# Performance work log

Hardware: AMD Instinct MI355X
Metric: run time of the kernel (lower is better)

Reference implementation:

```python
import jax, jax.numpy as jnp
import numpy as np

D_MODEL = 512
NUM_HEADS = 8
DEPTH = D_MODEL // NUM_HEADS


def setup_inputs() -> dict:
    key = jax.random.key(0)
    kx, kq, kk, kv, ko = jax.random.split(key, 5)
    scale = 1.0 / np.sqrt(D_MODEL)
    return {
        "x": jax.random.normal(kx, (4, 2048, D_MODEL), dtype=jnp.float32),
        "W_q": jax.random.normal(kq, (D_MODEL, D_MODEL), dtype=jnp.float32) * scale,
        "W_k": jax.random.normal(kk, (D_MODEL, D_MODEL), dtype=jnp.float32) * scale,
        "W_v": jax.random.normal(kv, (D_MODEL, D_MODEL), dtype=jnp.float32) * scale,
        "W_o": jax.random.normal(ko, (D_MODEL, D_MODEL), dtype=jnp.float32) * scale,
    }


def reference(x, W_q, W_k, W_v, W_o):
    B, S, _ = x.shape
    # nn.Linear with weight W: y = x @ W.T
    def split_heads(t):
        return t.reshape(B, S, NUM_HEADS, DEPTH).transpose(0, 2, 1, 3)  # [B,H,S,D]
    Q = split_heads(x @ W_q.T)
    K = split_heads(x @ W_k.T)
    V = split_heads(x @ W_v.T)
    b = -jnp.log(jnp.asarray(S, dtype=jnp.float32))  # -log(seq_len) bias
    inv_sqrt_dk = 1.0 / jnp.sqrt(jnp.asarray(DEPTH, dtype=jnp.float32))
    qk = jnp.einsum('bhqd,bhkd->bhqk', Q, K) * inv_sqrt_dk
    attn = jax.nn.sigmoid(qk + b)  # non-softmax sigmoid attention
    out = jnp.einsum('bhqk,bhkd->bhqd', attn, V)
    out = out.transpose(0, 2, 1, 3).reshape(B, S, D_MODEL)
    return out @ W_o.T
```

## Files before the change

### kernel.cpp

```cpp
#include <hip/hip_runtime.h>
#include <stdint.h>

typedef _Float16 f16x8 __attribute__((ext_vector_type(8)));
typedef _Float16 f16x4 __attribute__((ext_vector_type(4)));
typedef __fp16 h16x2 __attribute__((ext_vector_type(2)));
typedef float f32x4 __attribute__((ext_vector_type(4)));
typedef float f32x16 __attribute__((ext_vector_type(16)));

#define SEQ 2048
#define NHEADS 8

#define GLOAD_LDS16(gp, lp)                                                        \
  __builtin_amdgcn_global_load_lds(                                                \
      (const __attribute__((address_space(1))) void*)(uintptr_t)(const void*)(gp), \
      (__attribute__((address_space(3))) void*)(uintptr_t)(void*)(lp), 16, 0, 0)

#define DSR(dst, base, off) \
  asm volatile("ds_read_b128 %0, %1 offset:%c2" : "=v"(dst) : "v"(base), "i"(off))

#define WAIT_LGKM(n)                                         \
  do {                                                       \
    asm volatile("s_waitcnt lgkmcnt(%c0)" ::"i"(n) : "memory"); \
    __builtin_amdgcn_sched_barrier(0);                       \
  } while (0)

__device__ __forceinline__ void barrier_lds() {
  __builtin_amdgcn_s_waitcnt(0xc07f);
  __builtin_amdgcn_s_barrier();
}

__device__ __forceinline__ f16x4 pack4(float a, float b, float c, float d) {
  h16x2 lo = __builtin_amdgcn_cvt_pkrtz(a, b);
  h16x2 hi = __builtin_amdgcn_cvt_pkrtz(c, d);
  f16x4 o;
  o.x = (_Float16)lo.x; o.y = (_Float16)lo.y;
  o.z = (_Float16)hi.x; o.w = (_Float16)hi.y;
  return o;
}

__global__ void cvt_all_kernel(const float* __restrict__ x, const float* __restrict__ wq,
                               const float* __restrict__ wk, const float* __restrict__ wv,
                               const float* __restrict__ wo, _Float16* __restrict__ xh,
                               _Float16* __restrict__ wh) {
  int i = blockIdx.x * 256 + threadIdx.x;
  const float* src;
  _Float16* dst;
  int off;
  if (i < 1048576) {
    src = x; dst = xh; off = i;
  } else {
    int j = i - 1048576;
    int sel = j >> 16;
    off = j & 65535;
    src = (sel == 0) ? wq : (sel == 1) ? wk : (sel == 2) ? wv : wo;
    dst = wh + (size_t)sel * 262144;
  }
  float4 v = ((const float4*)src)[off];
  ((f16x4*)dst)[off] = pack4(v.x, v.y, v.z, v.w);
}

__device__ __forceinline__ void gemm_tile_bt(const _Float16* __restrict__ A,
                                             const _Float16* __restrict__ B,
                                             int m0, int n0,
                                             _Float16* lds,
                                             f32x4 (&acc)[4][4]) {
  const int tid = threadIdx.x;
  const int w = tid >> 6, lane = tid & 63;
  const int wr = w >> 1, wc = w & 1;
  const int lrow = lane & 15, q = lane >> 4;
  const int snb = w * 32 + (lane >> 3);
  const int scb = lane & 7;

#pragma unroll
  for (int i = 0; i < 4; ++i)
#pragma unroll
    for (int j = 0; j < 4; ++j)
#pragma unroll
      for (int r = 0; r < 4; ++r) acc[i][j][r] = 0.f;

#pragma unroll
  for (int t = 0; t < 4; ++t) {
    int n = snb + t * 8;
    int cbg = scb ^ (n & 7);
    GLOAD_LDS16(A + (size_t)(m0 + n) * 512 + cbg * 8, lds + (w * 32 + t * 8) * 64);
    GLOAD_LDS16(B + (size_t)(n0 + n) * 512 + cbg * 8, lds + 8192 + (w * 32 + t * 8) * 64);
  }

  for (int kt = 0; kt < 8; ++kt) {
    __syncthreads();
    if (kt < 7) {
      _Float16* nb = lds + ((kt + 1) & 1) * 16384;
#pragma unroll
      for (int t = 0; t < 4; ++t) {
        int n = snb + t * 8;
        int cbg = scb ^ (n & 7);
        GLOAD_LDS16(A + (size_t)(m0 + n) * 512 + (kt + 1) * 64 + cbg * 8, nb + (w * 32 + t * 8) * 64);
        GLOAD_LDS16(B + (size_t)(n0 + n) * 512 + (kt + 1) * 64 + cbg * 8, nb + 8192 + (w * 32 + t * 8) * 64);
      }
    }
    _Float16* As = lds + (kt & 1) * 16384;
    _Float16* Bs = As + 8192;

    f16x8 af[4][2], bfr[4][2];
#pragma unroll
    for (int i = 0; i < 4; ++i) {
      int m = wr * 64 + i * 16 + lrow;
#pragma unroll
      for (int kk = 0; kk < 2; ++kk) {
        int cb = (kk * 4 + q) ^ (m & 7);
        af[i][kk] = *(const f16x8*)(As + m * 64 + cb * 8);
      }
    }
#pragma unroll
    for (int j = 0; j < 4; ++j) {
      int n = wc * 64 + j * 16 + lrow;
#pragma unroll
      for (int kk = 0; kk < 2; ++kk) {
        int cb = (kk * 4 + q) ^ (n & 7);
        bfr[j][kk] = *(const f16x8*)(Bs + n * 64 + cb * 8);
      }
    }
#pragma unroll
    for (int i = 0; i < 4; ++i)
#pragma unroll
      for (int j = 0; j < 4; ++j) {
        acc[i][j] = __builtin_amdgcn_mfma_f32_16x16x32_f16(af[i][0], bfr[j][0], acc[i][j], 0, 0, 0);
        acc[i][j] = __builtin_amdgcn_mfma_f32_16x16x32_f16(af[i][1], bfr[j][1], acc[i][j], 0, 0, 0);
      }
  }
}

__global__ __launch_bounds__(256, 2) void qkv_kernel(
    const _Float16* __restrict__ xb, const _Float16* __restrict__ Wq,
    const _Float16* __restrict__ Wk, const _Float16* __restrict__ Wv,
    _Float16* __restrict__ Qo, _Float16* __restrict__ Ko, _Float16* __restrict__ Vto) {
  __shared__ _Float16 pool[32768];
  const int z = blockIdx.z;
  f32x4 acc[4][4];
  const int tid = threadIdx.x, w = tid >> 6, lane = tid & 63;
  const int wr = w >> 1, wc = w & 1, lcol = lane & 15, q = lane >> 4;

  if (z < 2) {
    const int m0 = blockIdx.y * 128;
    const int n0 = blockIdx.x * 128;
    gemm_tile_bt((z == 0) ? Wq : Wk, xb, m0, n0, pool, acc);
    _Float16* outp = (z == 0) ? Qo : Ko;
    __syncthreads();
#pragma unroll
    for (int i = 0; i < 4; ++i) {
      int cl = wr * 64 + i * 16 + q * 4;
#pragma unroll
      for (int j = 0; j < 4; ++j) {
        int s = wc * 64 + j * 16 + lcol;
        *(f16x4*)(pool + s * 136 + cl) =
            pack4(acc[i][j][0], acc[i][j][1], acc[i][j][2], acc[i][j][3]);
      }
    }
    __syncthreads();
#pragma unroll
    for (int it = 0; it < 16; ++it) {
      int srow = it * 8 + (tid >> 5);
      int ch = tid & 31;
      f16x4 v = *(const f16x4*)(pool + srow * 136 + ch * 4);
      *(f16x4*)(outp + (size_t)(n0 + srow) * 512 + m0 + ch * 4) = v;
    }
  } else {
    const int m0 = blockIdx.x * 128;
    const int n0 = blockIdx.y * 128;
    gemm_tile_bt(xb, Wv, m0, n0, pool, acc);
    const int bb = m0 >> 11, sl0 = m0 & 2047;
    __syncthreads();
#pragma unroll
    for (int i = 0; i < 4; ++i) {
      int s0 = wr * 64 + i * 16 + q * 4;
#pragma unroll
      for (int j = 0; j < 4; ++j) {
        int c = wc * 64 + j * 16 + lcol;
        *(f16x4*)(pool + c * 136 + s0) =
            pack4(acc[i][j][0], acc[i][j][1], acc[i][j][2], acc[i][j][3]);
      }
    }
    __syncthreads();
#pragma unroll
    for (int it = 0; it < 16; ++it) {
      int crow = it * 8 + (tid >> 5);
      int ch = tid & 31;
      int cg = n0 + crow, h = cg >> 6, d = cg & 63;
      f16x4 v = *(const f16x4*)(pool + crow * 136 + ch * 4);
      *(f16x4*)(Vto + ((size_t)((bb * NHEADS + h) * 64 + d)) * SEQ + sl0 + ch * 4) = v;
    }
  }
}

__device__ __forceinline__ void attn_window(
    f16x8 k0, f16x8 k1, f16x8 k2, f16x8 k3,
    f16x8 v00, f16x8 v01, f16x8 v10, f16x8 v11,
    const f16x8 (&qb)[4], const f32x16& z16, f32x16& o0, f32x16& o1) {
  const float c1 = 0.18033688011112042f;
  __builtin_amdgcn_s_setprio(1);
  f32x16 s = __builtin_amdgcn_mfma_f32_32x32x16_f16(k0, qb[0], z16, 0, 0, 0);
  s = __builtin_amdgcn_mfma_f32_32x32x16_f16(k1, qb[1], s, 0, 0, 0);
  s = __builtin_amdgcn_mfma_f32_32x32x16_f16(k2, qb[2], s, 0, 0, 0);
  s = __builtin_amdgcn_mfma_f32_32x32x16_f16(k3, qb[3], s, 0, 0, 0);
  __builtin_amdgcn_s_setprio(0);

  float p[16];
#pragma unroll
  for (int r = 0; r < 16; ++r) {
    float wp = __builtin_amdgcn_exp2f(__builtin_fmaf(s[r], c1, -1.0f));
    float e = wp * 0.0009765625f;
    p[r] = __builtin_fmaf(wp, __builtin_fmaf(e, e, -e), wp);
  }

  f16x8 pa0, pa1;
  {
    h16x2 a0 = __builtin_amdgcn_cvt_pkrtz(p[0], p[1]);
    h16x2 a1 = __builtin_amdgcn_cvt_pkrtz(p[2], p[3]);
    h16x2 a2 = __builtin_amdgcn_cvt_pkrtz(p[4], p[5]);
    h16x2 a3 = __builtin_amdgcn_cvt_pkrtz(p[6], p[7]);
    pa0[0] = (_Float16)a0.x; pa0[1] = (_Float16)a0.y;
    pa0[2] = (_Float16)a1.x; pa0[3] = (_Float16)a1.y;
    pa0[4] = (_Float16)a2.x; pa0[5] = (_Float16)a2.y;
    pa0[6] = (_Float16)a3.x; pa0[7] = (_Float16)a3.y;
    h16x2 b0 = __builtin_amdgcn_cvt_pkrtz(p[8], p[9]);
    h16x2 b1 = __builtin_amdgcn_cvt_pkrtz(p[10], p[11]);
    h16x2 b2 = __builtin_amdgcn_cvt_pkrtz(p[12], p[13]);
    h16x2 b3 = __builtin_amdgcn_cvt_pkrtz(p[14], p[15]);
    pa1[0] = (_Float16)b0.x; pa1[1] = (_Float16)b0.y;
    pa1[2] = (_Float16)b1.x; pa1[3] = (_Float16)b1.y;
    pa1[4] = (_Float16)b2.x; pa1[5] = (_Float16)b2.y;
    pa1[6] = (_Float16)b3.x; pa1[7] = (_Float16)b3.y;
  }

  __builtin_amdgcn_s_setprio(1);
  o0 = __builtin_amdgcn_mfma_f32_32x32x16_f16(pa0, v00, o0, 0, 0, 0);
  o1 = __builtin_amdgcn_mfma_f32_32x32x16_f16(pa0, v01, o1, 0, 0, 0);
  o0 = __builtin_amdgcn_mfma_f32_32x32x16_f16(pa1, v10, o0, 0, 0, 0);
  o1 = __builtin_amdgcn_mfma_f32_32x32x16_f16(pa1, v11, o1, 0, 0, 0);
  __builtin_amdgcn_s_setprio(0);
}

#define KT_BODY(BUFB, NBUFB, PF)                                              \
  {                                                                           \
    __syncthreads();                                                          \
    if (PF) {                                                                 \
      _Float16* nb = (_Float16*)((char*)lds + (NBUFB));                       \
      GLOAD_LDS16(kgb + koff[0], nb + (w * 16) * 64);                         \
      GLOAD_LDS16(kgb + koff[1], nb + (w * 16 + 8) * 64);                     \
      GLOAD_LDS16(vgb + voff[0], nb + 4096 + (w * 16) * 64);                  \
      GLOAD_LDS16(vgb + voff[1], nb + 4096 + (w * 16 + 8) * 64);              \
      kgb += 65536;                                                           \
      vgb += 128;                                                             \
    }                                                                         \
    f16x8 kA0, kA1, kA2, kA3, vA00, vA01, vA10, vA11;                         \
    f16x8 kB0, kB1, kB2, kB3, vB00, vB01, vB10, vB11;                         \
    DSR(kA0, kb0, (BUFB));                                                    \
    DSR(kA1, kb1, (BUFB));                                                    \
    DSR(kA2, kb2, (BUFB));                                                    \
    DSR(kA3, kb3, (BUFB));                                                    \
    DSR(vA00, pv00, (BUFB) + 8192);                                           \
    DSR(vA01, pv00, (BUFB) + 12288);                                          \
    DSR(vA10, pv01, (BUFB) + 8192);                                           \
    DSR(vA11, pv01, (BUFB) + 12288);                                          \
    DSR(kB0, kb0, (BUFB) + 4096);                                             \
    DSR(kB1, kb1, (BUFB) + 4096);                                             \
    DSR(kB2, kb2, (BUFB) + 4096);                                             \
    DSR(kB3, kb3, (BUFB) + 4096);                                             \
    DSR(vB00, pv10, (BUFB) + 8192);                                           \
    DSR(vB01, pv10, (BUFB) + 12288);                                          \
    DSR(vB10, pv11, (BUFB) + 8192);                                           \
    DSR(vB11, pv11, (BUFB) + 12288);                                          \
    WAIT_LGKM(8);                                                             \
    attn_window(kA0, kA1, kA2, kA3, vA00, vA01, vA10, vA11, qb, z16, oacc0, oacc1); \
    WAIT_LGKM(0);                                                             \
    attn_window(kB0, kB1, kB2, kB3, vB00, vB01, vB10, vB11, qb, z16, oacc0, oacc1); \
  }

__global__ __launch_bounds__(256, 2) void attn_kernel(
    const _Float16* __restrict__ Qw, const _Float16* __restrict__ Kw,
    const _Float16* __restrict__ Vtw, _Float16* __restrict__ Ow) {
  __shared__ _Float16 lds[16384];

  const int tid = threadIdx.x, w = tid >> 6, lane = tid & 63;
  const int q31 = lane & 31, hi = lane >> 5;

  const int L = blockIdx.x;
  const int xcd = L & 7, slot = L >> 3;
  const int bh = xcd * 4 + (slot >> 4), qt = slot & 15;
  const int b = bh >> 3, h = bh & 7;
  const int q0 = qt * 128;

  const _Float16* Qp = Qw + ((size_t)(b * SEQ + q0)) * 512 + h * 64;
  const _Float16* Kp = Kw + ((size_t)b * SEQ) * 512 + h * 64;
  const _Float16* Vp = Vtw + (size_t)bh * 64 * SEQ;

  const int l3 = lane >> 3, l7 = lane & 7;

  int koff[2], voff[2];
#pragma unroll
  for (int t = 0; t < 2; ++t) {
    int n = w * 16 + t * 8 + l3;
    int cbg = l7 ^ l3 ^ ((t & 1) << 2);
    koff[t] = n * 1024 + cbg * 16;
    voff[t] = n * 4096 + cbg * 16;
  }
  const char* kgb = (const char*)Kp;
  const char* vgb = (const char*)Vp;

  _Float16* Qs = lds + 8192;
#pragma unroll
  for (int t = 0; t < 4; ++t) {
    int n = w * 32 + t * 8 + l3;
    int cbg = l7 ^ l3 ^ ((t & 1) << 2);
    GLOAD_LDS16((const char*)Qp + n * 1024 + cbg * 16, Qs + (w * 32 + t * 8) * 64);
  }
  GLOAD_LDS16(kgb + koff[0], lds + (w * 16) * 64);
  GLOAD_LDS16(kgb + koff[1], lds + (w * 16 + 8) * 64);
  GLOAD_LDS16(vgb + voff[0], lds + 4096 + (w * 16) * 64);
  GLOAD_LDS16(vgb + voff[1], lds + 4096 + (w * 16 + 8) * 64);
  kgb += 65536;
  vgb += 128;
  __syncthreads();

  const int fq = (q31 & 7) ^ (((q31 >> 3) & 1) << 2);
  const int klp = (q31 & 3) | ((q31 & 4) << 1) | ((q31 & 8) >> 1) | (q31 & 16);
  const int fk = (klp & 7) ^ (((klp >> 3) & 1) << 2);

  f16x8 qb[4];
  const int qrow = w * 32 + q31;
#pragma unroll
  for (int s = 0; s < 4; ++s) {
    int cb = (s * 2 + hi) ^ fq;
    qb[s] = *(const f16x8*)(Qs + qrow * 64 + cb * 8);
  }

  const int kb0 = klp * 128 + (((0 * 2 + hi) ^ fk) << 4);
  const int kb1 = klp * 128 + (((1 * 2 + hi) ^ fk) << 4);
  const int kb2 = klp * 128 + (((2 * 2 + hi) ^ fk) << 4);
  const int kb3 = klp * 128 + (((3 * 2 + hi) ^ fk) << 4);
  const int pv00 = q31 * 128 + (((0 + 0 + hi) ^ fq) << 4);
  const int pv01 = q31 * 128 + (((0 + 2 + hi) ^ fq) << 4);
  const int pv10 = q31 * 128 + (((4 + 0 + hi) ^ fq) << 4);
  const int pv11 = q31 * 128 + (((4 + 2 + hi) ^ fq) << 4);

  f32x16 oacc0, oacc1, z16;
#pragma unroll
  for (int r = 0; r < 16; ++r) { z16[r] = 0.f; oacc0[r] = 0.f; oacc1[r] = 0.f; }

  for (int p = 0; p < 16; ++p) {
    KT_BODY(0, 16384, true);
    KT_BODY(16384, 0, (p < 15));
  }

  barrier_lds();
  _Float16* Ob = lds;
#pragma unroll
  for (int t = 0; t < 2; ++t) {
#pragma unroll
    for (int r = 0; r < 16; ++r) {
      int row = w * 32 + (r & 3) + ((r >> 2) << 3) + hi * 4;
      int d = t * 32 + q31;
      float v = (t == 0) ? oacc0[r] : oacc1[r];
      Ob[row * 72 + d] = (_Float16)(v * 0.0009765625f);
    }
  }
  barrier_lds();
#pragma unroll
  for (int it = 0; it < 8; ++it) {
    int row = it * 16 + (tid >> 4);
    int ch = tid & 15;
    f16x4 v = *(const f16x4*)(Ob + row * 72 + ch * 4);
    *(f16x4*)(Ow + (size_t)(b * SEQ + q0 + row) * 512 + h * 64 + ch * 4) = v;
  }
}

__global__ __launch_bounds__(256, 2) void oproj_kernel(
    const _Float16* __restrict__ A, const _Float16* __restrict__ Wo,
    float* __restrict__ out) {
  __shared__ _Float16 pool[32768];
  const int m0 = blockIdx.x * 128, n0 = blockIdx.y * 128;
  f32x4 acc[4][4];
  gemm_tile_bt(A, Wo, m0, n0, pool, acc);

  const int tid = threadIdx.x, w = tid >> 6, lane = tid & 63;
  const int wr = w >> 1, wc = w & 1, lcol = lane & 15, q = lane >> 4;
#pragma unroll
  for (int i = 0; i < 4; ++i) {
    int gm0 = m0 + wr * 64 + i * 16 + q * 4;
#pragma unroll
    for (int j = 0; j < 4; ++j) {
      int gn = n0 + wc * 64 + j * 16 + lcol;
#pragma unroll
      for (int r = 0; r < 4; ++r)
        out[(size_t)(gm0 + r) * 512 + gn] = acc[i][j][r];
    }
  }
}

extern "C" void kernel_launch(void* const* d_in, const int* in_sizes, int n_in,
                              void* d_out, int out_size, void* d_ws, size_t ws_size,
                              hipStream_t stream) {
  const float* x = (const float*)d_in[0];
  const float* Wq = (const float*)d_in[1];
  const float* Wk = (const float*)d_in[2];
  const float* Wv = (const float*)d_in[3];
  const float* Wo = (const float*)d_in[4];
  float* out = (float*)d_out;
  char* ws = (char*)d_ws;

  _Float16* xh = (_Float16*)(ws + 0);
  _Float16* wh = (_Float16*)(ws + 8388608);
  _Float16* Qw = (_Float16*)(ws + 10485760);
  _Float16* Kw = (_Float16*)(ws + 18874368);
  _Float16* Vtw = (_Float16*)(ws + 27262976);
  _Float16* Ow = (_Float16*)(ws + 35651584);

  _Float16* wqh = wh;
  _Float16* wkh = wh + 262144;
  _Float16* wvh = wh + 524288;
  _Float16* woh = wh + 786432;

  cvt_all_kernel<<<5120, 256, 0, stream>>>(x, Wq, Wk, Wv, Wo, xh, wh);
  qkv_kernel<<<dim3(64, 4, 3), 256, 0, stream>>>(xh, wqh, wkh, wvh, Qw, Kw, Vtw);
  attn_kernel<<<512, 256, 0, stream>>>(Qw, Kw, Vtw, Ow);
  oproj_kernel<<<dim3(64, 4), 256, 0, stream>>>(Ow, woh, out);
}
```

Baseline: 149.8 us.

## Load attention K/V tiles directly from global into registers, bypassing LDS

The attention kernel no longer stages K and V tiles through double-buffered LDS with block-wide barriers. Each wave now issues global_load_dwordx4 straight into registers for two ping-pong windows and waits on vmcnt. This removes the per-tile __syncthreads and the LDS round trip, and shrinks LDS use. In exchange every wave fetches its own K/V copy from global/L2, so redundant traffic rises across the 4 waves, and latency hiding now depends on how far ahead the register double-buffering prefetches.

```diff
diff --git a/kernel.cpp b/kernel.cpp
--- a/kernel.cpp
+++ b/kernel.cpp
@@ -15,19 +15,14 @@
       (const __attribute__((address_space(1))) void*)(uintptr_t)(const void*)(gp), \
       (__attribute__((address_space(3))) void*)(uintptr_t)(void*)(lp), 16, 0, 0)
 
-#define DSR(dst, base, off) \
-  asm volatile("ds_read_b128 %0, %1 offset:%c2" : "=v"(dst) : "v"(base), "i"(off))
-
-#define WAIT_LGKM(n)                                         \
-  do {                                                       \
-    asm volatile("s_waitcnt lgkmcnt(%c0)" ::"i"(n) : "memory"); \
-    __builtin_amdgcn_sched_barrier(0);                       \
+#define GLD16(dst, ptr, imm) \
+  asm volatile("global_load_dwordx4 %0, %1, off offset:%c2" : "=&v"(dst) : "v"(ptr), "i"(imm))
+
+#define VMW(n)                                                     \
+  do {                                                             \
+    asm volatile("s_waitcnt vmcnt(%c0)" ::"i"(n) : "memory");      \
+    __builtin_amdgcn_sched_barrier(0);                             \
   } while (0)
-
-__device__ __forceinline__ void barrier_lds() {
-  __builtin_amdgcn_s_waitcnt(0xc07f);
-  __builtin_amdgcn_s_barrier();
-}
 
 __device__ __forceinline__ f16x4 pack4(float a, float b, float c, float d) {
   h16x2 lo = __builtin_amdgcn_cvt_pkrtz(a, b);
@@ -192,16 +187,15 @@
   }
 }
 
-__device__ __forceinline__ void attn_window(
-    f16x8 k0, f16x8 k1, f16x8 k2, f16x8 k3,
-    f16x8 v00, f16x8 v01, f16x8 v10, f16x8 v11,
-    const f16x8 (&qb)[4], const f32x16& z16, f32x16& o0, f32x16& o1) {
+__device__ __forceinline__ void attn_window(const f16x8 (&ka)[4], const f16x8 (&vb)[4],
+                                            const f16x8 (&qb)[4], const f32x16& z16,
+                                            f32x16& o0, f32x16& o1) {
   const float c1 = 0.18033688011112042f;
   __builtin_amdgcn_s_setprio(1);
-  f32x16 s = __builtin_amdgcn_mfma_f32_32x32x16_f16(k0, qb[0], z16, 0, 0, 0);
-  s = __builtin_amdgcn_mfma_f32_32x32x16_f16(k1, qb[1], s, 0, 0, 0);
-  s = __builtin_amdgcn_mfma_f32_32x32x16_f16(k2, qb[2], s, 0, 0, 0);
-  s = __builtin_amdgcn_mfma_f32_32x32x16_f16(k3, qb[3], s, 0, 0, 0);
+  f32x16 s = __builtin_amdgcn_mfma_f32_32x32x16_f16(ka[0], qb[0], z16, 0, 0, 0);
+  s = __builtin_amdgcn_mfma_f32_32x32x16_f16(ka[1], qb[1], s, 0, 0, 0);
+  s = __builtin_amdgcn_mfma_f32_32x32x16_f16(ka[2], qb[2], s, 0, 0, 0);
+  s = __builtin_amdgcn_mfma_f32_32x32x16_f16(ka[3], qb[3], s, 0, 0, 0);
   __builtin_amdgcn_s_setprio(0);
 
   float p[16];
@@ -233,55 +227,34 @@
   }
 
   __builtin_amdgcn_s_setprio(1);
-  o0 = __builtin_amdgcn_mfma_f32_32x32x16_f16(pa0, v00, o0, 0, 0, 0);
-  o1 = __builtin_amdgcn_mfma_f32_32x32x16_f16(pa0, v01, o1, 0, 0, 0);
-  o0 = __builtin_amdgcn_mfma_f32_32x32x16_f16(pa1, v10, o0, 0, 0, 0);
-  o1 = __builtin_amdgcn_mfma_f32_32x32x16_f16(pa1, v11, o1, 0, 0, 0);
+  o0 = __builtin_amdgcn_mfma_f32_32x32x16_f16(pa0, vb[0], o0, 0, 0, 0);
+  o1 = __builtin_amdgcn_mfma_f32_32x32x16_f16(pa0, vb[1], o1, 0, 0, 0);
+  o0 = __builtin_amdgcn_mfma_f32_32x32x16_f16(pa1, vb[2], o0, 0, 0, 0);
+  o1 = __builtin_amdgcn_mfma_f32_32x32x16_f16(pa1, vb[3], o1, 0, 0, 0);
   __builtin_amdgcn_s_setprio(0);
 }
 
-#define KT_BODY(BUFB, NBUFB, PF)                                              \
-  {                                                                           \
-    __syncthreads();                                                          \
-    if (PF) {                                                                 \
-      _Float16* nb = (_Float16*)((char*)lds + (NBUFB));                       \
-      GLOAD_LDS16(kgb + koff[0], nb + (w * 16) * 64);                         \
-      GLOAD_LDS16(kgb + koff[1], nb + (w * 16 + 8) * 64);                     \
-      GLOAD_LDS16(vgb + voff[0], nb + 4096 + (w * 16) * 64);                  \
-      GLOAD_LDS16(vgb + voff[1], nb + 4096 + (w * 16 + 8) * 64);              \
-      kgb += 65536;                                                           \
-      vgb += 128;                                                             \
-    }                                                                         \
-    f16x8 kA0, kA1, kA2, kA3, vA00, vA01, vA10, vA11;                         \
-    f16x8 kB0, kB1, kB2, kB3, vB00, vB01, vB10, vB11;                         \
-    DSR(kA0, kb0, (BUFB));                                                    \
-    DSR(kA1, kb1, (BUFB));                                                    \
-    DSR(kA2, kb2, (BUFB));                                                    \
-    DSR(kA3, kb3, (BUFB));                                                    \
-    DSR(vA00, pv00, (BUFB) + 8192);                                           \
-    DSR(vA01, pv00, (BUFB) + 12288);                                          \
-    DSR(vA10, pv01, (BUFB) + 8192);                                           \
-    DSR(vA11, pv01, (BUFB) + 12288);                                          \
-    DSR(kB0, kb0, (BUFB) + 4096);                                             \
-    DSR(kB1, kb1, (BUFB) + 4096);                                             \
-    DSR(kB2, kb2, (BUFB) + 4096);                                             \
-    DSR(kB3, kb3, (BUFB) + 4096);                                             \
-    DSR(vB00, pv10, (BUFB) + 8192);                                           \
-    DSR(vB01, pv10, (BUFB) + 12288);                                          \
-    DSR(vB10, pv11, (BUFB) + 8192);                                           \
-    DSR(vB11, pv11, (BUFB) + 12288);                                          \
-    WAIT_LGKM(8);                                                             \
-    attn_window(kA0, kA1, kA2, kA3, vA00, vA01, vA10, vA11, qb, z16, oacc0, oacc1); \
-    WAIT_LGKM(0);                                                             \
-    attn_window(kB0, kB1, kB2, kB3, vB00, vB01, vB10, vB11, qb, z16, oacc0, oacc1); \
-  }
+#define ISSUE_WIN(KA, VB, KP, VP0, VP1) \
+  do {                                  \
+    GLD16(KA[0], KP, 0);                \
+    GLD16(KA[1], KP, 32);               \
+    GLD16(KA[2], KP, 64);               \
+    GLD16(KA[3], KP, 96);               \
+    GLD16(VB[0], VP0, 0);               \
+    GLD16(VB[1], VP1, 0);               \
+    GLD16(VB[2], VP0, 32);              \
+    GLD16(VB[3], VP1, 32);              \
+    KP += 65536;                        \
+    VP0 += 128;                         \
+    VP1 += 128;                         \
+  } while (0)
 
 __global__ __launch_bounds__(256, 2) void attn_kernel(
     const _Float16* __restrict__ Qw, const _Float16* __restrict__ Kw,
     const _Float16* __restrict__ Vtw, _Float16* __restrict__ Ow) {
-  __shared__ _Float16 lds[16384];
-
-  const int tid = threadIdx.x, w = tid >> 6, lane = tid & 63;
+  __shared__ _Float16 lds[9216];
+
+  const int tid = threadIdx.x, wv = tid >> 6, lane = tid & 63;
   const int q31 = lane & 31, hi = lane >> 5;
 
   const int L = blockIdx.x;
@@ -290,81 +263,56 @@
   const int b = bh >> 3, h = bh & 7;
   const int q0 = qt * 128;
 
-  const _Float16* Qp = Qw + ((size_t)(b * SEQ + q0)) * 512 + h * 64;
-  const _Float16* Kp = Kw + ((size_t)b * SEQ) * 512 + h * 64;
-  const _Float16* Vp = Vtw + (size_t)bh * 64 * SEQ;
-
-  const int l3 = lane >> 3, l7 = lane & 7;
-
-  int koff[2], voff[2];
+  const int klp = (q31 & 3) | ((q31 & 4) << 1) | ((q31 & 8) >> 1) | (q31 & 16);
+
+  const char* qp = (const char*)Qw +
+                   (size_t)(b * SEQ + q0 + wv * 32 + q31) * 1024 + h * 128 + hi * 16;
+  const char* kpA = (const char*)Kw + (size_t)(b * SEQ + klp) * 1024 + h * 128 + hi * 16;
+  const char* kpB = kpA + 32768;
+  const char* vp0A = (const char*)Vtw + (size_t)bh * 262144 + (size_t)q31 * 4096 + hi * 16;
+  const char* vp1A = vp0A + 32 * 4096;
+  const char* vp0B = vp0A + 64;
+  const char* vp1B = vp1A + 64;
+
+  f16x8 qb[4];
+  GLD16(qb[0], qp, 0);
+  GLD16(qb[1], qp, 32);
+  GLD16(qb[2], qp, 64);
+  GLD16(qb[3], qp, 96);
+
+  f16x8 kaA[4], vbA[4], kaB[4], vbB[4];
+  ISSUE_WIN(kaA, vbA, kpA, vp0A, vp1A);
+  ISSUE_WIN(kaB, vbB, kpB, vp0B, vp1B);
+
+  f32x16 oacc0, oacc1, z16;
+#pragma unroll
+  for (int r = 0; r < 16; ++r) { z16[r] = 0.f; oacc0[r] = 0.f; oacc1[r] = 0.f; }
+
+  for (int i = 0; i < 31; ++i) {
+    VMW(8);
+    attn_window(kaA, vbA, qb, z16, oacc0, oacc1);
+    ISSUE_WIN(kaA, vbA, kpA, vp0A, vp1A);
+    VMW(8);
+    attn_window(kaB, vbB, qb, z16, oacc0, oacc1);
+    ISSUE_WIN(kaB, vbB, kpB, vp0B, vp1B);
+  }
+  VMW(8);
+  attn_window(kaA, vbA, qb, z16, oacc0, oacc1);
+  VMW(0);
+  attn_window(kaB, vbB, qb, z16, oacc0, oacc1);
+
+  _Float16* Ob = lds;
 #pragma unroll
   for (int t = 0; t < 2; ++t) {
-    int n = w * 16 + t * 8 + l3;
-    int cbg = l7 ^ l3 ^ ((t & 1) << 2);
-    koff[t] = n * 1024 + cbg * 16;
-    voff[t] = n * 4096 + cbg * 16;
-  }
-  const char* kgb = (const char*)Kp;
-  const char* vgb = (const char*)Vp;
-
-  _Float16* Qs = lds + 8192;
-#pragma unroll
-  for (int t = 0; t < 4; ++t) {
-    int n = w * 32 + t * 8 + l3;
-    int cbg = l7 ^ l3 ^ ((t & 1) << 2);
-    GLOAD_LDS16((const char*)Qp + n * 1024 + cbg * 16, Qs + (w * 32 + t * 8) * 64);
-  }
-  GLOAD_LDS16(kgb + koff[0], lds + (w * 16) * 64);
-  GLOAD_LDS16(kgb + koff[1], lds + (w * 16 + 8) * 64);
-  GLOAD_LDS16(vgb + voff[0], lds + 4096 + (w * 16) * 64);
-  GLOAD_LDS16(vgb + voff[1], lds + 4096 + (w * 16 + 8) * 64);
-  kgb += 65536;
-  vgb += 128;
-  __syncthreads();
-
-  const int fq = (q31 & 7) ^ (((q31 >> 3) & 1) << 2);
-  const int klp = (q31 & 3) | ((q31 & 4) << 1) | ((q31 & 8) >> 1) | (q31 & 16);
-  const int fk = (klp & 7) ^ (((klp >> 3) & 1) << 2);
-
-  f16x8 qb[4];
-  const int qrow = w * 32 + q31;
-#pragma unroll
-  for (int s = 0; s < 4; ++s) {
-    int cb = (s * 2 + hi) ^ fq;
-    qb[s] = *(const f16x8*)(Qs + qrow * 64 + cb * 8);
-  }
-
-  const int kb0 = klp * 128 + (((0 * 2 + hi) ^ fk) << 4);
-  const int kb1 = klp * 128 + (((1 * 2 + hi) ^ fk) << 4);
-  const int kb2 = klp * 128 + (((2 * 2 + hi) ^ fk) << 4);
-  const int kb3 = klp * 128 + (((3 * 2 + hi) ^ fk) << 4);
-  const int pv00 = q31 * 128 + (((0 + 0 + hi) ^ fq) << 4);
-  const int pv01 = q31 * 128 + (((0 + 2 + hi) ^ fq) << 4);
-  const int pv10 = q31 * 128 + (((4 + 0 + hi) ^ fq) << 4);
-  const int pv11 = q31 * 128 + (((4 + 2 + hi) ^ fq) << 4);
-
-  f32x16 oacc0, oacc1, z16;
-#pragma unroll
-  for (int r = 0; r < 16; ++r) { z16[r] = 0.f; oacc0[r] = 0.f; oacc1[r] = 0.f; }
-
-  for (int p = 0; p < 16; ++p) {
-    KT_BODY(0, 16384, true);
-    KT_BODY(16384, 0, (p < 15));
-  }
-
-  barrier_lds();
-  _Float16* Ob = lds;
-#pragma unroll
-  for (int t = 0; t < 2; ++t) {
 #pragma unroll
     for (int r = 0; r < 16; ++r) {
-      int row = w * 32 + (r & 3) + ((r >> 2) << 3) + hi * 4;
+      int row = wv * 32 + (r & 3) + ((r >> 2) << 3) + hi * 4;
       int d = t * 32 + q31;
       float v = (t == 0) ? oacc0[r] : oacc1[r];
       Ob[row * 72 + d] = (_Float16)(v * 0.0009765625f);
     }
   }
-  barrier_lds();
+  __syncthreads();
 #pragma unroll
   for (int it = 0; it < 8; ++it) {
     int row = it * 16 + (tid >> 4);
```

Result: slower. 222.1 us (+48.3%).
